# Performance work log

Hardware: AMD Instinct MI355X
Metric: run time of the kernel (lower is better)

## Reference

```python
import jax, jax.numpy as jnp
import numpy as np

N_NODES = 100000
HIDDEN = 128
N_CLASS = 10
N_EDGES = 1600000


def setup_inputs() -> dict:
    key = jax.random.key(0)
    ks = jax.random.split(key, 8)
    s = 1.0 / np.sqrt(HIDDEN)
    return {
        "edge_index": jax.random.randint(ks[0], (2, N_EDGES), 0, N_NODES, dtype=jnp.int32),
        "embedding": jax.random.normal(ks[1], (N_NODES, HIDDEN), jnp.float32),
        "W1": jax.random.normal(ks[2], (HIDDEN, HIDDEN), jnp.float32) * s,
        "b1": jnp.zeros((HIDDEN,), jnp.float32),
        "W2": jax.random.normal(ks[3], (HIDDEN, HIDDEN), jnp.float32) * s,
        "b2": jnp.zeros((HIDDEN,), jnp.float32),
        "W_out": jax.random.normal(ks[4], (HIDDEN, N_CLASS), jnp.float32) * s,
        "b_out": jnp.zeros((N_CLASS,), jnp.float32),
    }


def reference(edge_index, embedding, W1, b1, W2, b2, W_out, b_out):
    N = embedding.shape[0]
    # PyG GCNConv: add self-loops, symmetric normalization D^-1/2 (A+I) D^-1/2
    loops = jnp.arange(N, dtype=edge_index.dtype)
    src = jnp.concatenate([edge_index[0], loops])  # message sources
    dst = jnp.concatenate([edge_index[1], loops])  # aggregation targets
    deg = jax.ops.segment_sum(jnp.ones_like(dst, jnp.float32), dst, num_segments=N)
    inv_sqrt = jnp.where(deg > 0, jax.lax.rsqrt(jnp.maximum(deg, 1.0)), 0.0)
    norm = inv_sqrt[src] * inv_sqrt[dst]  # [E+N]

    x = embedding  # forward ignores input x, uses learned embedding table
    for W, b in ((W1, b1), (W2, b2)):
        h = x @ W                                      # [N, H]
        msg = h[src] * norm[:, None]                   # gather + scale, [E+N, H]
        agg = jax.ops.segment_sum(msg, dst, num_segments=N)
        x = jax.nn.relu(agg + b)
    return x @ W_out + b_out
```

## Files before the change

### kernel.cpp

```cpp
#include <hip/hip_runtime.h>
#include <hip/hip_bf16.h>

#define HID 128
#define NCLASS 10
#define PCHUNK 8192
#define HB 256

typedef unsigned int uint;
typedef unsigned short ushort;
typedef __attribute__((ext_vector_type(8))) __bf16 bf16x8;
typedef __attribute__((ext_vector_type(4))) float f32x4;

__device__ __forceinline__ uint bf16rne(float x) {
    uint u = __float_as_uint(x);
    return (u + 0x7FFFu + ((u >> 16) & 1u)) >> 16;
}
__device__ __forceinline__ uint pack2(float e0, float e1) {
    return bf16rne(e0) | (bf16rne(e1) << 16);
}
__device__ __forceinline__ void unpack2(uint w, float& lo, float& hi) {
    lo = __uint_as_float(w << 16);
    hi = __uint_as_float(w & 0xFFFF0000u);
}
__device__ __forceinline__ void split2(float e0, float e1, uint& h, uint& l) {
    uint h0 = bf16rne(e0), h1 = bf16rne(e1);
    float r0 = e0 - __uint_as_float(h0 << 16);
    float r1 = e1 - __uint_as_float(h1 << 16);
    h = h0 | (h1 << 16);
    l = bf16rne(r0) | (bf16rne(r1) << 16);
}
__device__ __forceinline__ bf16x8 as_bf16x8(uint4 u) {
    return __builtin_bit_cast(bf16x8, u);
}
__device__ __forceinline__ void unpack8(uint4 u, float* f) {
    unpack2(u.x, f[0], f[1]); unpack2(u.y, f[2], f[3]);
    unpack2(u.z, f[4], f[5]); unpack2(u.w, f[6], f[7]);
}

__device__ __forceinline__ void pack_w_body(const float* __restrict__ W,
                                            uint* __restrict__ hi, uint* __restrict__ lo,
                                            int slot, int l) {
    const int s = slot >> 3, t = slot & 7;
    const int kb = s * 32 + (l >> 4) * 8, n = t * 16 + (l & 15);
    float f[8];
#pragma unroll
    for (int j = 0; j < 8; ++j) f[j] = W[(kb + j) * HID + n];
    uint4 h, lo4;
    split2(f[0], f[1], h.x, lo4.x);
    split2(f[2], f[3], h.y, lo4.y);
    split2(f[4], f[5], h.z, lo4.z);
    split2(f[6], f[7], h.w, lo4.w);
    const int fo = (slot * 64 + l) * 4;
    *(uint4*)(hi + fo) = h;
    *(uint4*)(lo + fo) = lo4;
}

__global__ __launch_bounds__(256) void hist_pack_kernel(
        const int* __restrict__ dst, int* __restrict__ bcnt, int E, int NB,
        const float* __restrict__ W1, uint* __restrict__ W1hi, uint* __restrict__ W1lo,
        const float* __restrict__ W2, uint* __restrict__ W2hi, uint* __restrict__ W2lo) {
    __shared__ int h[400];
    const int t = threadIdx.x;
    if ((int)blockIdx.x < HB) {
        const int ech = (E + HB - 1) / HB;
        const int e0 = blockIdx.x * ech;
        const int e1 = min(E, e0 + ech);
        for (int i = t; i < NB; i += 256) h[i] = 0;
        __syncthreads();
        for (int e = e0 + t; e < e1; e += 256) atomicAdd(&h[dst[e] >> 8], 1);
        __syncthreads();
        for (int i = t; i < NB; i += 256)
            if (h[i]) atomicAdd(&bcnt[i], h[i]);
    } else {
        const int pb = blockIdx.x - HB;
        const int slot = (pb & 7) * 4 + (t >> 6);
        const int l = t & 63;
        if (pb < 8) pack_w_body(W1, W1hi, W1lo, slot, l);
        else        pack_w_body(W2, W2hi, W2lo, slot, l);
    }
}

template <bool FP32IN>
__device__ __forceinline__ void gemm_body_mfma(
        const float* __restrict__ Xf, const uint* __restrict__ Xhi,
        const uint* __restrict__ Wphi, const uint* __restrict__ Wplo,
        ushort* __restrict__ HS, int N, int bidx, int tid) {
    const int wv = tid >> 6;
    const int l = tid & 63;
    const int q = l >> 4;
    const int cm = l & 15;
    const long rowbase = (long)bidx * 128 + wv * 32;

    bf16x8 bhi[2][4], blo[2][4];
#pragma unroll
    for (int rt = 0; rt < 2; ++rt) {
        const long row = rowbase + rt * 16 + cm;
        const long rc = row < N ? row : (N - 1);
#pragma unroll
        for (int s = 0; s < 4; ++s) {
            if (FP32IN) {
                const float* xp = Xf + rc * HID + s * 32 + q * 8;
                const float4 a0 = ((const float4*)xp)[0];
                const float4 a1 = ((const float4*)xp)[1];
                uint4 h, lo4;
                split2(a0.x, a0.y, h.x, lo4.x);
                split2(a0.z, a0.w, h.y, lo4.y);
                split2(a1.x, a1.y, h.z, lo4.z);
                split2(a1.z, a1.w, h.w, lo4.w);
                bhi[rt][s] = as_bf16x8(h);
                blo[rt][s] = as_bf16x8(lo4);
            } else {
                const long o = rc * (HID / 2) + s * 16 + q * 4;
                bhi[rt][s] = as_bf16x8(*(const uint4*)(Xhi + o));
            }
        }
    }

    f32x4 acc[2][8];
#pragma unroll
    for (int rt = 0; rt < 2; ++rt)
#pragma unroll
        for (int t = 0; t < 8; ++t) acc[rt][t] = (f32x4)0.0f;

#pragma unroll
    for (int s = 0; s < 4; ++s) {
#pragma unroll
        for (int t = 0; t < 8; ++t) {
            const int fo = ((s * 8 + t) * 64 + l) * 4;
            const bf16x8 whi = as_bf16x8(*(const uint4*)(Wphi + fo));
            const bf16x8 wlo = as_bf16x8(*(const uint4*)(Wplo + fo));
#pragma unroll
            for (int rt = 0; rt < 2; ++rt) {
                acc[rt][t] = __builtin_amdgcn_mfma_f32_16x16x32_bf16(whi, bhi[rt][s], acc[rt][t], 0, 0, 0);
                if (FP32IN)
                    acc[rt][t] = __builtin_amdgcn_mfma_f32_16x16x32_bf16(whi, blo[rt][s], acc[rt][t], 0, 0, 0);
                acc[rt][t] = __builtin_amdgcn_mfma_f32_16x16x32_bf16(wlo, bhi[rt][s], acc[rt][t], 0, 0, 0);
            }
        }
    }

#pragma unroll
    for (int rt = 0; rt < 2; ++rt) {
        const long row = rowbase + rt * 16 + cm;
        if (row < N) {
#pragma unroll
            for (int t = 0; t < 8; ++t) {
                uint2 o;
                o.x = pack2(acc[rt][t][0], acc[rt][t][1]);
                o.y = pack2(acc[rt][t][2], acc[rt][t][3]);
                *(uint2*)&HS[row * HID + t * 16 + q * 4] = o;
            }
        }
    }
}

__global__ __launch_bounds__(256) void gemm1_part_kernel(
        const float* __restrict__ emb, const uint* __restrict__ Wphi,
        const uint* __restrict__ Wplo, ushort* __restrict__ HS, int N,
        const int* __restrict__ src, const int* __restrict__ dst,
        int* __restrict__ gcursor, uint* __restrict__ staged, int E, int PB, int NB) {
    __shared__ int hist[400], lbase[400], loff[400];
    const int t = threadIdx.x;
    if ((int)blockIdx.x >= PB) {
        gemm_body_mfma<true>(emb, nullptr, Wphi, Wplo, HS, N, blockIdx.x - PB, t);
        return;
    }
    const int e0 = blockIdx.x * PCHUNK;
    for (int i = t; i < NB; i += 256) { hist[i] = 0; loff[i] = 0; }
    __syncthreads();
#pragma unroll
    for (int j = 0; j < PCHUNK / 256; ++j) {
        const int e = e0 + j * 256 + t;
        if (e < E) atomicAdd(&hist[dst[e] >> 8], 1);
    }
    __syncthreads();
    for (int b = t; b < NB; b += 256)
        if (hist[b] > 0) lbase[b] = atomicAdd(&gcursor[b], hist[b]);
    __syncthreads();
#pragma unroll
    for (int j = 0; j < PCHUNK / 256; ++j) {
        const int e = e0 + j * 256 + t;
        if (e < E) {
            const int d = dst[e];
            const int b = d >> 8;
            const int pos = lbase[b] + atomicAdd(&loff[b], 1);
            staged[pos] = (uint)src[e] | ((uint)(d & 255) << 17);
        }
    }
}

__global__ __launch_bounds__(256) void gemm2_kernel(
        const uint* __restrict__ Xhi, const uint* __restrict__ Wphi,
        const uint* __restrict__ Wplo, ushort* __restrict__ HS, int N) {
    gemm_body_mfma<false>(nullptr, Xhi, Wphi, Wplo, HS, N, blockIdx.x, threadIdx.x);
}

__global__ __launch_bounds__(512) void scan_buckets_kernel(const int* __restrict__ bcnt,
                                                           int* bbase, int* gcursor,
                                                           int* rps, int NB, int E, int N) {
    __shared__ int sh[512];
    const int t = threadIdx.x;
    const int v = (t < NB) ? bcnt[t] : 0;
    sh[t] = v;
    __syncthreads();
    for (int off = 1; off < 512; off <<= 1) {
        int x = (t >= off) ? sh[t - off] : 0;
        __syncthreads();
        sh[t] += x;
        __syncthreads();
    }
    const int excl = sh[t] - v;
    if (t < NB) { bbase[t] = excl; gcursor[t] = excl; }
    if (t == NB - 1) bbase[NB] = excl + v;
    if (t == 0) rps[N] = E;
}

__global__ __launch_bounds__(256) void fill_bucket_kernel(
        const uint* __restrict__ staged, const int* __restrict__ bbase,
        int* __restrict__ rps, float* __restrict__ invs, int* __restrict__ col, int N) {
    __shared__ int h[256], cur[256], sh[256];
    const int b = blockIdx.x, t = threadIdx.x;
    const int w0 = bbase[b], w1 = bbase[b + 1];
    const int base0 = b << 8;
    h[t] = 0;
    __syncthreads();
    for (int i = w0 + t; i < w1; i += 256) atomicAdd(&h[staged[i] >> 17], 1);
    __syncthreads();
    const int my = h[t];
    sh[t] = my;
    __syncthreads();
    for (int off = 1; off < 256; off <<= 1) {
        int x = (t >= off) ? sh[t - off] : 0;
        __syncthreads();
        sh[t] += x;
        __syncthreads();
    }
    const int start = w0 + sh[t] - my;
    cur[t] = start;
    const int node = base0 + t;
    if (node < N) {
        rps[node] = start;
        invs[node] = rsqrtf((float)my + 1.0f);
    }
    __syncthreads();
    for (int i = w0 + t; i < w1; i += 256) {
        const uint u = staged[i];
        const int p = atomicAdd(&cur[u >> 17], 1);
        col[p] = (int)(u & 0x1FFFFu);
    }
}

__global__ __launch_bounds__(256) void pull_relu_kernel(
        const int* __restrict__ rps, const int* __restrict__ col,
        const uint* __restrict__ HS, const float* __restrict__ invs,
        const float* __restrict__ b, uint* __restrict__ Xhi, int N) {
    const int g = blockIdx.x * 256 + threadIdx.x;
    const int node = g >> 4;
    if (node >= N) return;
    const int lane = g & 15;
    const int p = rps[node];
    const int d = rps[node + 1] - p;
    const uint4* H4 = (const uint4*)HS;

    const float sn = invs[node];
    float acc[8];
    {
        float f[8];
        unpack8(H4[(size_t)node * 16 + lane], f);
#pragma unroll
        for (int j = 0; j < 8; ++j) acc[j] = f[j] * sn;
    }
    int i = 0;
    for (; i + 8 <= d; i += 8) {
        int s[8];
#pragma unroll
        for (int k = 0; k < 8; ++k) s[k] = col[p + i + k];
        uint4 a[8];
#pragma unroll
        for (int k = 0; k < 8; ++k) a[k] = H4[(size_t)s[k] * 16 + lane];
        float w[8];
#pragma unroll
        for (int k = 0; k < 8; ++k) w[k] = invs[s[k]];
#pragma unroll
        for (int k = 0; k < 8; ++k) {
            float f[8];
            unpack8(a[k], f);
#pragma unroll
            for (int j = 0; j < 8; ++j) acc[j] += f[j] * w[k];
        }
    }
    for (; i + 2 <= d; i += 2) {
        const int s0 = col[p + i], s1 = col[p + i + 1];
        const uint4 a0 = H4[(size_t)s0 * 16 + lane];
        const uint4 a1 = H4[(size_t)s1 * 16 + lane];
        const float w0 = invs[s0], w1 = invs[s1];
        float f0[8], f1[8];
        unpack8(a0, f0); unpack8(a1, f1);
#pragma unroll
        for (int j = 0; j < 8; ++j) acc[j] += f0[j] * w0;
#pragma unroll
        for (int j = 0; j < 8; ++j) acc[j] += f1[j] * w1;
    }
    if (i < d) {
        const int s0 = col[p + i];
        const float w0 = invs[s0];
        float f[8];
        unpack8(H4[(size_t)s0 * 16 + lane], f);
#pragma unroll
        for (int j = 0; j < 8; ++j) acc[j] += f[j] * w0;
    }
    float x[8];
#pragma unroll
    for (int j = 0; j < 8; ++j)
        x[j] = sn * fmaxf(acc[j] * sn + b[lane * 8 + j], 0.0f);
    uint4 h;
    h.x = pack2(x[0], x[1]); h.y = pack2(x[2], x[3]);
    h.z = pack2(x[4], x[5]); h.w = pack2(x[6], x[7]);
    *(uint4*)&Xhi[(size_t)node * 64 + lane * 4] = h;
}

__global__ __launch_bounds__(256) void pull_out_kernel(
        const int* __restrict__ rps, const int* __restrict__ col,
        const uint* __restrict__ HS, const float* __restrict__ invs,
        const float* __restrict__ b2, const float* __restrict__ Wout,
        const float* __restrict__ bout, float* __restrict__ OUT, int N) {
    __shared__ float Wd[320 * 4];
    for (int t = threadIdx.x; t < 320; t += 256) {
        const int c = t >> 5, rem = t & 31, j4 = rem >> 4, l = rem & 15;
        const int k0 = l * 8 + j4 * 4;
        float4 w;
        w.x = Wout[(k0 + 0) * NCLASS + c];
        w.y = Wout[(k0 + 1) * NCLASS + c];
        w.z = Wout[(k0 + 2) * NCLASS + c];
        w.w = Wout[(k0 + 3) * NCLASS + c];
        ((float4*)Wd)[(c * 2 + j4) * 16 + l] = w;
    }
    __syncthreads();

    const int g = blockIdx.x * 256 + threadIdx.x;
    const int node = g >> 4;
    if (node >= N) return;
    const int lane = g & 15;
    const int p = rps[node];
    const int d = rps[node + 1] - p;
    const uint4* H4 = (const uint4*)HS;

    float acc[8];
    unpack8(H4[(size_t)node * 16 + lane], acc);
    int i = 0;
    for (; i + 8 <= d; i += 8) {
        int s[8];
#pragma unroll
        for (int k = 0; k < 8; ++k) s[k] = col[p + i + k];
        uint4 a[8];
#pragma unroll
        for (int k = 0; k < 8; ++k) a[k] = H4[(size_t)s[k] * 16 + lane];
#pragma unroll
        for (int k = 0; k < 8; ++k) {
            float f[8];
            unpack8(a[k], f);
#pragma unroll
            for (int j = 0; j < 8; ++j) acc[j] += f[j];
        }
    }
    for (; i + 2 <= d; i += 2) {
        const int s0 = col[p + i], s1 = col[p + i + 1];
        const uint4 a0 = H4[(size_t)s0 * 16 + lane];
        const uint4 a1 = H4[(size_t)s1 * 16 + lane];
        float f0[8], f1[8];
        unpack8(a0, f0); unpack8(a1, f1);
#pragma unroll
        for (int j = 0; j < 8; ++j) acc[j] += f0[j] + f1[j];
    }
    if (i < d) {
        const int s0 = col[p + i];
        float f[8];
        unpack8(H4[(size_t)s0 * 16 + lane], f);
#pragma unroll
        for (int j = 0; j < 8; ++j) acc[j] += f[j];
    }
    const float sn = invs[node];
    float x[8];
#pragma unroll
    for (int j = 0; j < 8; ++j) x[j] = fmaxf(acc[j] * sn + b2[lane * 8 + j], 0.0f);

    const float4 xv0 = make_float4(x[0], x[1], x[2], x[3]);
    const float4 xv1 = make_float4(x[4], x[5], x[6], x[7]);
    const float4* Wd4 = (const float4*)Wd;
    float res = 0.0f;
#pragma unroll
    for (int c = 0; c < NCLASS; ++c) {
        const float4 w0 = Wd4[(c * 2 + 0) * 16 + lane];
        const float4 w1 = Wd4[(c * 2 + 1) * 16 + lane];
        float s = xv0.x * w0.x + xv0.y * w0.y + xv0.z * w0.z + xv0.w * w0.w
                + xv1.x * w1.x + xv1.y * w1.y + xv1.z * w1.z + xv1.w * w1.w;
        s += __shfl_xor(s, 1, 16);
        s += __shfl_xor(s, 2, 16);
        s += __shfl_xor(s, 4, 16);
        s += __shfl_xor(s, 8, 16);
        if (lane == c) res = s;
    }
    if (lane < NCLASS) OUT[(size_t)node * NCLASS + lane] = res + bout[lane];
}

extern "C" void kernel_launch(void* const* d_in, const int* in_sizes, int n_in,
                              void* d_out, int out_size, void* d_ws, size_t ws_size,
                              hipStream_t stream) {
    const int* ei     = (const int*)d_in[0];
    const float* emb  = (const float*)d_in[1];
    const float* W1   = (const float*)d_in[2];
    const float* b1   = (const float*)d_in[3];
    const float* W2   = (const float*)d_in[4];
    const float* b2   = (const float*)d_in[5];
    const float* Wout = (const float*)d_in[6];
    const float* bout = (const float*)d_in[7];
    float* out        = (float*)d_out;

    const int E = in_sizes[0] / 2;
    const int N = in_sizes[1] / HID;
    const int* src = ei;
    const int* dst = ei + E;
    (void)ws_size; (void)n_in; (void)out_size;

    const int GB = (N + 127) / 128;
    const int NB = (N + 255) >> 8;
    const int PB = (E + PCHUNK - 1) / PCHUNK;

    char* ws = (char*)d_ws;
    size_t off = 0;
    auto alloc = [&](size_t bytes) {
        void* p = ws + off;
        off = (off + bytes + 4095) & ~(size_t)4095;
        return p;
    };
    int*   bcnt    = (int*)alloc(512 * 4);
    int*   bbase   = (int*)alloc(512 * 4);
    int*   gcursor = (int*)alloc(512 * 4);
    int*   rps     = (int*)alloc((size_t)(N + 1) * 4);
    float* invs    = (float*)alloc((size_t)N * 4);
    int*   col     = (int*)alloc((size_t)E * 4);
    uint*  staged  = (uint*)alloc((size_t)E * 4);
    uint*  Wp1hi   = (uint*)alloc(HID * HID * 2);
    uint*  Wp1lo   = (uint*)alloc(HID * HID * 2);
    uint*  Wp2hi   = (uint*)alloc(HID * HID * 2);
    uint*  Wp2lo   = (uint*)alloc(HID * HID * 2);
    uint*  HS      = (uint*)alloc((size_t)N * HID * 2);
    uint*  X1hi    = (uint*)alloc((size_t)N * HID * 2);

    hipMemsetAsync(bcnt, 0, 512 * 4, stream);
    hist_pack_kernel<<<HB + 16, 256, 0, stream>>>(dst, bcnt, E, NB,
                                                  W1, Wp1hi, Wp1lo, W2, Wp2hi, Wp2lo);
    scan_buckets_kernel<<<1, 512, 0, stream>>>(bcnt, bbase, gcursor, rps, NB, E, N);
    gemm1_part_kernel<<<PB + GB, 256, 0, stream>>>(emb, Wp1hi, Wp1lo, (ushort*)HS, N,
                                                   src, dst, gcursor, staged, E, PB, NB);
    fill_bucket_kernel<<<NB, 256, 0, stream>>>(staged, bbase, rps, invs, col, N);

    pull_relu_kernel<<<((size_t)N * 16 + 255) / 256, 256, 0, stream>>>(
        rps, col, HS, invs, b1, X1hi, N);

    gemm2_kernel<<<GB, 256, 0, stream>>>(X1hi, Wp2hi, Wp2lo, (ushort*)HS, N);
    pull_out_kernel<<<((size_t)N * 16 + 255) / 256, 256, 0, stream>>>(
        rps, col, HS, invs, b2, Wout, bout, out, N);
}
```

Baseline: 337.8 us.

## Store hidden features in column-sliced layout for cache-local gathers

Changes the bf16 hidden-feature layout from row-major to 8 column slices of 16 features each. The GEMM outputs and inputs are rewritten to match, and the gather kernels now process one slice per block, so each slice's gathered working set (about 3.2 MB) can stay in L2 during random neighbor gathers. The fused layer-2 pull plus output projection is split into a sliced pull kernel and a separate output GEMM kernel. This adds one extra intermediate buffer write and read and one more launch, and each slice pass re-reads rps, col and invs.

```diff
diff --git a/kernel.cpp b/kernel.cpp
--- a/kernel.cpp
+++ b/kernel.cpp
@@ -84,7 +84,7 @@
 __device__ __forceinline__ void gemm_body_mfma(
         const float* __restrict__ Xf, const uint* __restrict__ Xhi,
         const uint* __restrict__ Wphi, const uint* __restrict__ Wplo,
-        ushort* __restrict__ HS, int N, int bidx, int tid) {
+        uint* __restrict__ HS, int N, int bidx, int tid) {
     const int wv = tid >> 6;
     const int l = tid & 63;
     const int q = l >> 4;
@@ -110,8 +110,8 @@
                 bhi[rt][s] = as_bf16x8(h);
                 blo[rt][s] = as_bf16x8(lo4);
             } else {
-                const long o = rc * (HID / 2) + s * 16 + q * 4;
-                bhi[rt][s] = as_bf16x8(*(const uint4*)(Xhi + o));
+                const size_t o = ((size_t)(2 * s + (q >> 1)) * N + rc) * 2 + (q & 1);
+                bhi[rt][s] = as_bf16x8(((const uint4*)Xhi)[o]);
             }
         }
     }
@@ -148,7 +148,7 @@
                 uint2 o;
                 o.x = pack2(acc[rt][t][0], acc[rt][t][1]);
                 o.y = pack2(acc[rt][t][2], acc[rt][t][3]);
-                *(uint2*)&HS[row * HID + t * 16 + q * 4] = o;
+                *(uint2*)&HS[((size_t)t * N + row) * 8 + q * 2] = o;
             }
         }
     }
@@ -156,7 +156,7 @@
 
 __global__ __launch_bounds__(256) void gemm1_part_kernel(
         const float* __restrict__ emb, const uint* __restrict__ Wphi,
-        const uint* __restrict__ Wplo, ushort* __restrict__ HS, int N,
+        const uint* __restrict__ Wplo, uint* __restrict__ HS, int N,
         const int* __restrict__ src, const int* __restrict__ dst,
         int* __restrict__ gcursor, uint* __restrict__ staged, int E, int PB, int NB) {
     __shared__ int hist[400], lbase[400], loff[400];
@@ -191,7 +191,7 @@
 
 __global__ __launch_bounds__(256) void gemm2_kernel(
         const uint* __restrict__ Xhi, const uint* __restrict__ Wphi,
-        const uint* __restrict__ Wplo, ushort* __restrict__ HS, int N) {
+        const uint* __restrict__ Wplo, uint* __restrict__ HS, int N) {
     gemm_body_mfma<false>(nullptr, Xhi, Wphi, Wplo, HS, N, blockIdx.x, threadIdx.x);
 }
 
@@ -250,25 +250,30 @@
     }
 }
 
-__global__ __launch_bounds__(256) void pull_relu_kernel(
+template <bool LAYER1>
+__global__ __launch_bounds__(256) void pull_sliced_kernel(
         const int* __restrict__ rps, const int* __restrict__ col,
-        const uint* __restrict__ HS, const float* __restrict__ invs,
-        const float* __restrict__ b, uint* __restrict__ Xhi, int N) {
-    const int g = blockIdx.x * 256 + threadIdx.x;
-    const int node = g >> 4;
+        const uint* __restrict__ Hs, const float* __restrict__ invs,
+        const float* __restrict__ bias, uint* __restrict__ Xout, int N) {
+    const int slice = blockIdx.x & 7;
+    const int chunk = blockIdx.x >> 3;
+    const int t = threadIdx.x;
+    const int node = chunk * 128 + (t >> 1);
     if (node >= N) return;
-    const int lane = g & 15;
+    const int half = t & 1;
+    const uint4* H4 = (const uint4*)Hs;
+    const size_t sbase = (size_t)slice * N;
+
     const int p = rps[node];
     const int d = rps[node + 1] - p;
-    const uint4* H4 = (const uint4*)HS;
-
     const float sn = invs[node];
+
     float acc[8];
     {
         float f[8];
-        unpack8(H4[(size_t)node * 16 + lane], f);
-#pragma unroll
-        for (int j = 0; j < 8; ++j) acc[j] = f[j] * sn;
+        unpack8(H4[(sbase + node) * 2 + half], f);
+#pragma unroll
+        for (int j = 0; j < 8; ++j) acc[j] = LAYER1 ? f[j] * sn : f[j];
     }
     int i = 0;
     for (; i + 8 <= d; i += 8) {
@@ -277,52 +282,53 @@
         for (int k = 0; k < 8; ++k) s[k] = col[p + i + k];
         uint4 a[8];
 #pragma unroll
-        for (int k = 0; k < 8; ++k) a[k] = H4[(size_t)s[k] * 16 + lane];
+        for (int k = 0; k < 8; ++k) a[k] = H4[(sbase + s[k]) * 2 + half];
         float w[8];
-#pragma unroll
-        for (int k = 0; k < 8; ++k) w[k] = invs[s[k]];
+        if (LAYER1) {
+#pragma unroll
+            for (int k = 0; k < 8; ++k) w[k] = invs[s[k]];
+        }
 #pragma unroll
         for (int k = 0; k < 8; ++k) {
             float f[8];
             unpack8(a[k], f);
 #pragma unroll
-            for (int j = 0; j < 8; ++j) acc[j] += f[j] * w[k];
+            for (int j = 0; j < 8; ++j) acc[j] += LAYER1 ? f[j] * w[k] : f[j];
         }
     }
     for (; i + 2 <= d; i += 2) {
         const int s0 = col[p + i], s1 = col[p + i + 1];
-        const uint4 a0 = H4[(size_t)s0 * 16 + lane];
-        const uint4 a1 = H4[(size_t)s1 * 16 + lane];
-        const float w0 = invs[s0], w1 = invs[s1];
+        const uint4 a0 = H4[(sbase + s0) * 2 + half];
+        const uint4 a1 = H4[(sbase + s1) * 2 + half];
+        float w0 = 1.0f, w1 = 1.0f;
+        if (LAYER1) { w0 = invs[s0]; w1 = invs[s1]; }
         float f0[8], f1[8];
         unpack8(a0, f0); unpack8(a1, f1);
 #pragma unroll
-        for (int j = 0; j < 8; ++j) acc[j] += f0[j] * w0;
-#pragma unroll
-        for (int j = 0; j < 8; ++j) acc[j] += f1[j] * w1;
+        for (int j = 0; j < 8; ++j) acc[j] += LAYER1 ? (f0[j] * w0 + f1[j] * w1) : (f0[j] + f1[j]);
     }
     if (i < d) {
         const int s0 = col[p + i];
-        const float w0 = invs[s0];
+        const float w0 = LAYER1 ? invs[s0] : 1.0f;
         float f[8];
-        unpack8(H4[(size_t)s0 * 16 + lane], f);
-#pragma unroll
-        for (int j = 0; j < 8; ++j) acc[j] += f[j] * w0;
+        unpack8(H4[(sbase + s0) * 2 + half], f);
+#pragma unroll
+        for (int j = 0; j < 8; ++j) acc[j] += LAYER1 ? f[j] * w0 : f[j];
     }
     float x[8];
 #pragma unroll
-    for (int j = 0; j < 8; ++j)
-        x[j] = sn * fmaxf(acc[j] * sn + b[lane * 8 + j], 0.0f);
+    for (int j = 0; j < 8; ++j) {
+        const float r = fmaxf(acc[j] * sn + bias[slice * 16 + half * 8 + j], 0.0f);
+        x[j] = LAYER1 ? sn * r : r;
+    }
     uint4 h;
     h.x = pack2(x[0], x[1]); h.y = pack2(x[2], x[3]);
     h.z = pack2(x[4], x[5]); h.w = pack2(x[6], x[7]);
-    *(uint4*)&Xhi[(size_t)node * 64 + lane * 4] = h;
-}
-
-__global__ __launch_bounds__(256) void pull_out_kernel(
-        const int* __restrict__ rps, const int* __restrict__ col,
-        const uint* __restrict__ HS, const float* __restrict__ invs,
-        const float* __restrict__ b2, const float* __restrict__ Wout,
+    ((uint4*)Xout)[(sbase + node) * 2 + half] = h;
+}
+
+__global__ __launch_bounds__(256) void out_gemm_kernel(
+        const uint* __restrict__ X2s, const float* __restrict__ Wout,
         const float* __restrict__ bout, float* __restrict__ OUT, int N) {
     __shared__ float Wd[320 * 4];
     for (int t = threadIdx.x; t < 320; t += 256) {
@@ -341,48 +347,9 @@
     const int node = g >> 4;
     if (node >= N) return;
     const int lane = g & 15;
-    const int p = rps[node];
-    const int d = rps[node + 1] - p;
-    const uint4* H4 = (const uint4*)HS;
-
-    float acc[8];
-    unpack8(H4[(size_t)node * 16 + lane], acc);
-    int i = 0;
-    for (; i + 8 <= d; i += 8) {
-        int s[8];
-#pragma unroll
-        for (int k = 0; k < 8; ++k) s[k] = col[p + i + k];
-        uint4 a[8];
-#pragma unroll
-        for (int k = 0; k < 8; ++k) a[k] = H4[(size_t)s[k] * 16 + lane];
-#pragma unroll
-        for (int k = 0; k < 8; ++k) {
-            float f[8];
-            unpack8(a[k], f);
-#pragma unroll
-            for (int j = 0; j < 8; ++j) acc[j] += f[j];
-        }
-    }
-    for (; i + 2 <= d; i += 2) {
-        const int s0 = col[p + i], s1 = col[p + i + 1];
-        const uint4 a0 = H4[(size_t)s0 * 16 + lane];
-        const uint4 a1 = H4[(size_t)s1 * 16 + lane];
-        float f0[8], f1[8];
-        unpack8(a0, f0); unpack8(a1, f1);
-#pragma unroll
-        for (int j = 0; j < 8; ++j) acc[j] += f0[j] + f1[j];
-    }
-    if (i < d) {
-        const int s0 = col[p + i];
-        float f[8];
-        unpack8(H4[(size_t)s0 * 16 + lane], f);
-#pragma unroll
-        for (int j = 0; j < 8; ++j) acc[j] += f[j];
-    }
-    const float sn = invs[node];
+    const uint4 u = ((const uint4*)X2s)[((size_t)(lane >> 1) * N + node) * 2 + (lane & 1)];
     float x[8];
-#pragma unroll
-    for (int j = 0; j < 8; ++j) x[j] = fmaxf(acc[j] * sn + b2[lane * 8 + j], 0.0f);
+    unpack8(u, x);
 
     const float4 xv0 = make_float4(x[0], x[1], x[2], x[3]);
     const float4 xv1 = make_float4(x[4], x[5], x[6], x[7]);
@@ -425,6 +392,7 @@
     const int GB = (N + 127) / 128;
     const int NB = (N + 255) >> 8;
     const int PB = (E + PCHUNK - 1) / PCHUNK;
+    const int NC = (N + 127) / 128;
 
     char* ws = (char*)d_ws;
     size_t off = 0;
@@ -446,19 +414,20 @@
     uint*  Wp2lo   = (uint*)alloc(HID * HID * 2);
     uint*  HS      = (uint*)alloc((size_t)N * HID * 2);
     uint*  X1hi    = (uint*)alloc((size_t)N * HID * 2);
+    uint*  X2s     = (uint*)alloc((size_t)N * HID * 2);
 
     hipMemsetAsync(bcnt, 0, 512 * 4, stream);
     hist_pack_kernel<<<HB + 16, 256, 0, stream>>>(dst, bcnt, E, NB,
                                                   W1, Wp1hi, Wp1lo, W2, Wp2hi, Wp2lo);
     scan_buckets_kernel<<<1, 512, 0, stream>>>(bcnt, bbase, gcursor, rps, NB, E, N);
-    gemm1_part_kernel<<<PB + GB, 256, 0, stream>>>(emb, Wp1hi, Wp1lo, (ushort*)HS, N,
+    gemm1_part_kernel<<<PB + GB, 256, 0, stream>>>(emb, Wp1hi, Wp1lo, HS, N,
                                                    src, dst, gcursor, staged, E, PB, NB);
     fill_bucket_kernel<<<NB, 256, 0, stream>>>(staged, bbase, rps, invs, col, N);
 
-    pull_relu_kernel<<<((size_t)N * 16 + 255) / 256, 256, 0, stream>>>(
-        rps, col, HS, invs, b1, X1hi, N);
-
-    gemm2_kernel<<<GB, 256, 0, stream>>>(X1hi, Wp2hi, Wp2lo, (ushort*)HS, N);
-    pull_out_kernel<<<((size_t)N * 16 + 255) / 256, 256, 0, stream>>>(
-        rps, col, HS, invs, b2, Wout, bout, out, N);
-}
+    pull_sliced_kernel<true><<<NC * 8, 256, 0, stream>>>(rps, col, HS, invs, b1, X1hi, N);
+
+    gemm2_kernel<<<GB, 256, 0, stream>>>(X1hi, Wp2hi, Wp2lo, HS, N);
+    pull_sliced_kernel<false><<<NC * 8, 256, 0, stream>>>(rps, col, HS, invs, b2, X2s, N);
+
+    out_gemm_kernel<<<((size_t)N * 16 + 255) / 256, 256, 0, stream>>>(X2s, Wout, bout, out, N);
+}
```

Result: slower. 433.4 us (+28.3%).
